# Optimization experiments

Measured on AMD Instinct MI355X. Metric: run time of the kernel, lower is better.

Reference implementation:

```python
import jax, jax.numpy as jnp
import numpy as np

B, T, I, H, FUT = 16384, 50, 6, 128, 30


def setup_inputs() -> dict:
    key = jax.random.key(0)
    ks = jax.random.split(key, 10)
    bound = 1.0 / np.sqrt(H)
    u = lambda k, shape: jax.random.uniform(k, shape, jnp.float32, -bound, bound)
    return {
        "history": jax.random.normal(ks[0], (B, T, I), jnp.float32),
        # GRU weights (PyTorch layout: gates stacked [r, z, n])
        "w_ih": u(ks[1], (3 * H, I)),
        "w_hh": u(ks[2], (3 * H, H)),
        "b_ih": u(ks[3], (3 * H,)),
        "b_hh": u(ks[4], (3 * H,)),
        # MLP head: Linear(H,H) -> ReLU -> Linear(H,I)
        "w1": u(ks[5], (H, H)),
        "b1": u(ks[6], (H,)),
        "w2": u(ks[7], (I, H)),
        "b2": u(ks[8], (I,)),
    }


def _gru_cell(h, x, w_ih, w_hh, b_ih, b_hh):
    # PyTorch GRU cell: gates ordered r, z, n
    gi = x @ w_ih.T + b_ih          # (B, 3H)
    gh = h @ w_hh.T + b_hh          # (B, 3H)
    i_r, i_z, i_n = jnp.split(gi, 3, axis=-1)
    h_r, h_z, h_n = jnp.split(gh, 3, axis=-1)
    r = jax.nn.sigmoid(i_r + h_r)
    z = jax.nn.sigmoid(i_z + h_z)
    n = jnp.tanh(i_n + r * h_n)
    return (1.0 - z) * n + z * h


def reference(history, w_ih, w_hh, b_ih, b_hh, w1, b1, w2, b2):
    # --- encode history: scan GRU over time ---
    h0 = jnp.zeros((history.shape[0], H), history.dtype)

    def enc_step(h, x_t):
        return _gru_cell(h, x_t, w_ih, w_hh, b_ih, b_hh), None

    h_last, _ = jax.lax.scan(enc_step, h0, jnp.swapaxes(history, 0, 1))  # (B, H)

    def head(h):
        return jax.nn.relu(h @ w1.T + b1) @ w2.T + b2  # (B, I)

    def dec_step(carry, _):
        h, x = carry
        h = _gru_cell(h, x, w_ih, w_hh, b_ih, b_hh)
        x = head(h)
        return (h, x), x

    x0 = history[:, -1]  # (B, I)
    _, preds = jax.lax.scan(dec_step, (h_last, x0), None, length=FUT)  # (FUT, B, I)
    return jnp.swapaxes(preds, 0, 1)  # (B, FUT, I)
```

## Files before the change

kernel.cpp:

```cpp
#include <hip/hip_runtime.h>

typedef _Float16 half8 __attribute__((ext_vector_type(8)));
typedef _Float16 half4 __attribute__((ext_vector_type(4)));
typedef float f32x4 __attribute__((ext_vector_type(4)));
typedef int int4v __attribute__((ext_vector_type(4)));

#define ROWS 64
#define HP 136
#define HBUFSZ (ROWS * HP)
#define LOG2E 1.442695041f
#define MFMA(a,b,c) __builtin_amdgcn_mfma_f32_16x16x32_f16((a),(b),(c),0,0,0)

__global__ __launch_bounds__(512, 2)
void traj_gru(const float* __restrict__ history,
              const float* __restrict__ w_ih, const float* __restrict__ w_hh,
              const float* __restrict__ b_ih, const float* __restrict__ b_hh,
              const float* __restrict__ w1, const float* __restrict__ b1,
              const float* __restrict__ w2, const float* __restrict__ b2,
              float* __restrict__ out)
{
    __shared__ __align__(16) _Float16 hbuf[2 * HBUFSZ];
    __shared__ __align__(16) _Float16 xhist[50 * ROWS * 6];
    __shared__ __align__(16) _Float16 xdec[ROWS * 8];
    __shared__ __align__(16) _Float16 w2f[4 * 4 * 16 * 8];

    const int tid  = threadIdx.x;
    const int wave = tid >> 6;
    const int lane = tid & 63;
    const int ln16 = lane & 15;
    const int q    = lane >> 4;
    const int sw   = ln16 & 3;
    const int rowbase = blockIdx.x * ROWS;
    const int dbase = wave * 16;
    const int bblk  = wave >> 1;
    const int colin = ((wave & 1) << 4) | ln16;

    for (int i = tid; i < 2 * HBUFSZ; i += 512) hbuf[i] = (_Float16)0;
    for (int i = tid; i < ROWS * 8; i += 512) xdec[i] = (_Float16)0;
    for (int i = tid; i < 4 * 4 * 16 * 8; i += 512) w2f[i] = (_Float16)0;
    __syncthreads();
    for (int idx = tid; idx < ROWS * 300; idx += 512) {
        int r = idx / 300, rem = idx - r * 300;
        int t = rem / 6, c = rem - t * 6;
        xhist[(t * ROWS + r) * 6 + c] = (_Float16)history[(rowbase + r) * 300 + rem];
    }
    if (tid < ROWS) xdec[tid * 8 + 6] = (_Float16)1.0f;
    for (int idx = tid; idx < 6 * 128; idx += 512) {
        int n = idx >> 7, k = idx & 127;
        int kt = k >> 5, qq = (k >> 3) & 3, j = k & 7;
        w2f[((kt * 4 + qq) * 16 + n) * 8 + j] = (_Float16)w2[n * 128 + k];
    }

    half8 Wg[3][4];
    #pragma unroll
    for (int g = 0; g < 3; ++g) {
        float sc = (g < 2) ? -LOG2E : -2.0f * LOG2E;
        #pragma unroll
        for (int kt = 0; kt < 4; ++kt) {
            const float* p = w_hh + (g * 128 + dbase + ln16) * 128 + kt * 32 + q * 8;
            half8 v;
            #pragma unroll
            for (int j = 0; j < 8; ++j) v[j] = (_Float16)(p[j] * sc);
            Wg[g][kt] = v;
        }
    }
    half8 Wx[3];
    #pragma unroll
    for (int g = 0; g < 3; ++g) {
        float sc = (g < 2) ? -LOG2E : -2.0f * LOG2E;
        half8 v;
        #pragma unroll
        for (int j = 0; j < 8; ++j) v[j] = (_Float16)0.0f;
        if (q == 0) {
            #pragma unroll
            for (int j = 0; j < 6; ++j) v[j] = (_Float16)(w_ih[(g * 128 + dbase + ln16) * 6 + j] * sc);
        }
        Wx[g] = v;
    }
    f32x4 brr, brz, bin, bhn;
    #pragma unroll
    for (int i = 0; i < 4; ++i) {
        int d = dbase + q * 4 + i;
        brr[i] = (b_ih[d]       + b_hh[d]      ) * (-LOG2E);
        brz[i] = (b_ih[128 + d] + b_hh[128 + d]) * (-LOG2E);
        bin[i] = b_ih[256 + d] * (-2.0f * LOG2E);
        bhn[i] = b_hh[256 + d] * (-2.0f * LOG2E);
    }
    half8 Bw1[4];
    #pragma unroll
    for (int kt = 0; kt < 4; ++kt) {
        const float* p = w1 + (dbase + ln16) * 128 + kt * 32 + q * 8;
        half8 v;
        #pragma unroll
        for (int j = 0; j < 8; ++j) v[j] = (_Float16)p[j];
        Bw1[kt] = v;
    }
    const float b1r = b1[dbase + ln16];
    const float b2r = (ln16 < 6) ? b2[ln16] : 0.0f;

    float hp[4][4] = {};

    __syncthreads();

    auto gru_step = [&](int p, int t, bool enc) {
        const _Float16* hb = hbuf + p * HBUFSZ;
        _Float16*       hn = hbuf + (p ^ 1) * HBUFSZ;
        half8 Bf[2][4], Bx[2];
        f32x4 ar[2], az[2], ahh[2], an[2];

        auto loadB = [&](int c, int buf) {
            const _Float16* rp = hb + (c * 16 + ln16) * HP;
            #pragma unroll
            for (int kt = 0; kt < 4; ++kt)
                Bf[buf][kt] = *(const half8*)(rp + kt * 32 + q * 8);
            if (enc) {
                const int* xi = (const int*)xhist;
                int base = (t * ROWS + c * 16 + ln16) * 3;
                int4v d = { xi[base], xi[base + 1], xi[base + 2], 0x3C00 };
                Bx[buf] = __builtin_bit_cast(half8, d);
            } else {
                Bx[buf] = *(const half8*)(xdec + (c * 16 + ln16) * 8);
            }
        };
        auto mfmas = [&](int buf) {
            f32x4 r = brr, z = brz, hh = bhn, n = bin;
            #pragma unroll
            for (int kt = 0; kt < 4; ++kt) {
                r  = MFMA(Wg[0][kt], Bf[buf][kt], r);
                z  = MFMA(Wg[1][kt], Bf[buf][kt], z);
                hh = MFMA(Wg[2][kt], Bf[buf][kt], hh);
            }
            r = MFMA(Wx[0], Bx[buf], r);
            z = MFMA(Wx[1], Bx[buf], z);
            n = MFMA(Wx[2], Bx[buf], n);
            ar[buf] = r; az[buf] = z; ahh[buf] = hh; an[buf] = n;
        };
        auto gates = [&](int c, int cb) {
            half4 hv;
            #pragma unroll
            for (int i = 0; i < 4; ++i) {
                float r = __builtin_amdgcn_rcpf(1.0f + __builtin_amdgcn_exp2f(ar[cb][i]));
                float z = __builtin_amdgcn_rcpf(1.0f + __builtin_amdgcn_exp2f(az[cb][i]));
                float tt = an[cb][i] + r * ahh[cb][i];
                float n = 2.0f * __builtin_amdgcn_rcpf(1.0f + __builtin_amdgcn_exp2f(tt)) - 1.0f;
                float h = n + z * (hp[c][i] - n);
                hp[c][i] = h;
                hv[i] = (_Float16)h;
            }
            *(half4*)(hn + (c * 16 + ln16) * HP + dbase + q * 4) = hv;
        };

        loadB(0, 0); mfmas(0);
        #pragma unroll
        for (int c = 0; c < 4; ++c) {
            const int cb = c & 1;
            if (c < 3) { loadB(c + 1, cb ^ 1); mfmas(cb ^ 1); }
            gates(c, cb);
        }
        __syncthreads();
    };

    auto head_step = [&](int f, int p) {
        const _Float16* hb = hbuf + p * HBUFSZ;
        _Float16*       a1 = hbuf + (p ^ 1) * HBUFSZ;
        half8 Ah[2][4];
        f32x4 aa[2];
        auto loadA = [&](int c, int buf) {
            const _Float16* rp = hb + (c * 16 + ln16) * HP;
            #pragma unroll
            for (int kt = 0; kt < 4; ++kt)
                Ah[buf][kt] = *(const half8*)(rp + kt * 32 + q * 8);
        };
        auto mfh = [&](int buf) {
            f32x4 a = {0,0,0,0};
            #pragma unroll
            for (int kt = 0; kt < 4; ++kt) a = MFMA(Ah[buf][kt], Bw1[kt], a);
            aa[buf] = a;
        };
        auto relu4 = [&](int c, int cb) {
            #pragma unroll
            for (int i = 0; i < 4; ++i) {
                float v = aa[cb][i] + b1r;
                v = v > 0.0f ? v : 0.0f;
                a1[(c * 16 + q * 4 + i) * HP + ((bblk ^ i) << 5) + colin] = (_Float16)v;
            }
        };
        loadA(0, 0); mfh(0);
        #pragma unroll
        for (int c = 0; c < 4; ++c) {
            const int cb = c & 1;
            if (c < 3) { loadA(c + 1, cb ^ 1); mfh(cb ^ 1); }
            relu4(c, cb);
        }
        __syncthreads();
        if (wave < 4) {
            const _Float16* rp = a1 + (wave * 16 + ln16) * HP;
            f32x4 o = {0,0,0,0};
            #pragma unroll
            for (int kt = 0; kt < 4; ++kt) {
                half8 Aa = *(const half8*)(rp + ((kt ^ sw) << 5) + q * 8);
                half8 Bw = *(const half8*)&w2f[((kt * 4 + q) * 16 + ln16) * 8];
                o = MFMA(Aa, Bw, o);
            }
            if (ln16 < 6) {
                #pragma unroll
                for (int i = 0; i < 4; ++i) {
                    int row = wave * 16 + q * 4 + i;
                    float v = o[i] + b2r;
                    out[(rowbase + row) * 180 + f * 6 + ln16] = v;
                    xdec[row * 8 + ln16] = (_Float16)v;
                }
            }
        }
        __syncthreads();
    };

    int p = 0;
    #pragma unroll 1
    for (int t = 0; t < 50; ++t) { gru_step(p, t, true); p ^= 1; }
    #pragma unroll 1
    for (int f = 0; f < 30; ++f) {
        gru_step(p, f == 0 ? 49 : 0, f == 0);
        p ^= 1;
        head_step(f, p);
    }
}

extern "C" void kernel_launch(void* const* d_in, const int* in_sizes, int n_in,
                              void* d_out, int out_size, void* d_ws, size_t ws_size,
                              hipStream_t stream) {
    (void)in_sizes; (void)n_in; (void)d_ws; (void)ws_size; (void)out_size;
    traj_gru<<<dim3(16384 / ROWS), dim3(512), 0, stream>>>(
        (const float*)d_in[0], (const float*)d_in[1], (const float*)d_in[2],
        (const float*)d_in[3], (const float*)d_in[4], (const float*)d_in[5],
        (const float*)d_in[6], (const float*)d_in[7], (const float*)d_in[8],
        (float*)d_out);
}
```

Before: 273.8 us.

## Split GRU work 2x4 over batch halves and hidden groups, stage w1 in LDS

Waves are regrouped so each one handles half the batch rows (two 16-row chunks) and a 32-wide hidden slice (two M-tiles), in place of all 64 rows for a 16-wide slice. This halves the LDS reads of the hidden state per wave and doubles the reuse of each loaded B fragment across two weight tiles. The gate biases are folded into the constant-1 column of the input MFMA so the accumulators start at zero. w1 now lives in LDS and is reloaded every head step rather than held in registers. In exchange, per-thread weight registers double (Wg is now 24 half8) and there is less software pipelining across chunks, which at launch bounds (512,2) may cause spills or lower occupancy.

```diff
diff --git a/kernel.cpp b/kernel.cpp
--- a/kernel.cpp
+++ b/kernel.cpp
@@ -23,17 +23,16 @@
     __shared__ __align__(16) _Float16 xhist[50 * ROWS * 6];
     __shared__ __align__(16) _Float16 xdec[ROWS * 8];
     __shared__ __align__(16) _Float16 w2f[4 * 4 * 16 * 8];
+    __shared__ __align__(16) _Float16 w1f[4 * 4 * 128 * 8];
 
     const int tid  = threadIdx.x;
     const int wave = tid >> 6;
     const int lane = tid & 63;
     const int ln16 = lane & 15;
     const int q    = lane >> 4;
-    const int sw   = ln16 & 3;
+    const int bh   = wave >> 2;
+    const int dg   = wave & 3;
     const int rowbase = blockIdx.x * ROWS;
-    const int dbase = wave * 16;
-    const int bblk  = wave >> 1;
-    const int colin = ((wave & 1) << 4) | ln16;
 
     for (int i = tid; i < 2 * HBUFSZ; i += 512) hbuf[i] = (_Float16)0;
     for (int i = tid; i < ROWS * 8; i += 512) xdec[i] = (_Float16)0;
@@ -50,55 +49,63 @@
         int kt = k >> 5, qq = (k >> 3) & 3, j = k & 7;
         w2f[((kt * 4 + qq) * 16 + n) * 8 + j] = (_Float16)w2[n * 128 + k];
     }
-
-    half8 Wg[3][4];
+    for (int idx = tid; idx < 16384; idx += 512) {
+        int j = idx & 7, d = (idx >> 3) & 127, fq = idx >> 10;
+        int kt = fq >> 2, qq = fq & 3;
+        w1f[idx] = (_Float16)w1[d * 128 + kt * 32 + qq * 8 + j];
+    }
+
+    half8 Wg[3][4][2];
     #pragma unroll
     for (int g = 0; g < 3; ++g) {
         float sc = (g < 2) ? -LOG2E : -2.0f * LOG2E;
         #pragma unroll
-        for (int kt = 0; kt < 4; ++kt) {
-            const float* p = w_hh + (g * 128 + dbase + ln16) * 128 + kt * 32 + q * 8;
-            half8 v;
-            #pragma unroll
-            for (int j = 0; j < 8; ++j) v[j] = (_Float16)(p[j] * sc);
-            Wg[g][kt] = v;
-        }
-    }
-    half8 Wx[3];
+        for (int mt = 0; mt < 2; ++mt) {
+            #pragma unroll
+            for (int kt = 0; kt < 4; ++kt) {
+                const float* p = w_hh + (g * 128 + dg * 32 + mt * 16 + ln16) * 128 + kt * 32 + q * 8;
+                half8 v;
+                #pragma unroll
+                for (int j = 0; j < 8; ++j) v[j] = (_Float16)(p[j] * sc);
+                Wg[g][kt][mt] = v;
+            }
+        }
+    }
+    half8 Wx[3][2];
     #pragma unroll
     for (int g = 0; g < 3; ++g) {
         float sc = (g < 2) ? -LOG2E : -2.0f * LOG2E;
-        half8 v;
-        #pragma unroll
-        for (int j = 0; j < 8; ++j) v[j] = (_Float16)0.0f;
-        if (q == 0) {
-            #pragma unroll
-            for (int j = 0; j < 6; ++j) v[j] = (_Float16)(w_ih[(g * 128 + dbase + ln16) * 6 + j] * sc);
-        }
-        Wx[g] = v;
-    }
-    f32x4 brr, brz, bin, bhn;
+        #pragma unroll
+        for (int mt = 0; mt < 2; ++mt) {
+            half8 v;
+            #pragma unroll
+            for (int j = 0; j < 8; ++j) v[j] = (_Float16)0.0f;
+            if (q == 0) {
+                int d = dg * 32 + mt * 16 + ln16;
+                #pragma unroll
+                for (int j = 0; j < 6; ++j) v[j] = (_Float16)(w_ih[(g * 128 + d) * 6 + j] * sc);
+                float bias;
+                if      (g == 0) bias = b_ih[d]       + b_hh[d];
+                else if (g == 1) bias = b_ih[128 + d] + b_hh[128 + d];
+                else             bias = b_ih[256 + d];
+                v[6] = (_Float16)(bias * sc);
+            }
+            Wx[g][mt] = v;
+        }
+    }
+    f32x4 bhn[2];
     #pragma unroll
-    for (int i = 0; i < 4; ++i) {
-        int d = dbase + q * 4 + i;
-        brr[i] = (b_ih[d]       + b_hh[d]      ) * (-LOG2E);
-        brz[i] = (b_ih[128 + d] + b_hh[128 + d]) * (-LOG2E);
-        bin[i] = b_ih[256 + d] * (-2.0f * LOG2E);
-        bhn[i] = b_hh[256 + d] * (-2.0f * LOG2E);
-    }
-    half8 Bw1[4];
-    #pragma unroll
-    for (int kt = 0; kt < 4; ++kt) {
-        const float* p = w1 + (dbase + ln16) * 128 + kt * 32 + q * 8;
-        half8 v;
-        #pragma unroll
-        for (int j = 0; j < 8; ++j) v[j] = (_Float16)p[j];
-        Bw1[kt] = v;
-    }
-    const float b1r = b1[dbase + ln16];
+    for (int mt = 0; mt < 2; ++mt)
+        #pragma unroll
+        for (int i = 0; i < 4; ++i)
+            bhn[mt][i] = b_hh[256 + dg * 32 + mt * 16 + q * 4 + i] * (-2.0f * LOG2E);
+
+    float b1rv[2];
+    b1rv[0] = b1[dg * 32 + ln16];
+    b1rv[1] = b1[dg * 32 + 16 + ln16];
     const float b2r = (ln16 < 6) ? b2[ln16] : 0.0f;
 
-    float hp[4][4] = {};
+    float hp[2][2][4] = {};
 
     __syncthreads();
 
@@ -106,101 +113,110 @@
         const _Float16* hb = hbuf + p * HBUFSZ;
         _Float16*       hn = hbuf + (p ^ 1) * HBUFSZ;
         half8 Bf[2][4], Bx[2];
-        f32x4 ar[2], az[2], ahh[2], an[2];
-
-        auto loadB = [&](int c, int buf) {
+
+        auto loadB = [&](int c2) {
+            int c = 2 * bh + c2;
             const _Float16* rp = hb + (c * 16 + ln16) * HP;
             #pragma unroll
             for (int kt = 0; kt < 4; ++kt)
-                Bf[buf][kt] = *(const half8*)(rp + kt * 32 + q * 8);
+                Bf[c2][kt] = *(const half8*)(rp + kt * 32 + q * 8);
             if (enc) {
                 const int* xi = (const int*)xhist;
                 int base = (t * ROWS + c * 16 + ln16) * 3;
-                int4v d = { xi[base], xi[base + 1], xi[base + 2], 0x3C00 };
-                Bx[buf] = __builtin_bit_cast(half8, d);
+                int4v dv = { xi[base], xi[base + 1], xi[base + 2], 0x3C00 };
+                Bx[c2] = __builtin_bit_cast(half8, dv);
             } else {
-                Bx[buf] = *(const half8*)(xdec + (c * 16 + ln16) * 8);
+                Bx[c2] = *(const half8*)(xdec + (c * 16 + ln16) * 8);
             }
         };
-        auto mfmas = [&](int buf) {
-            f32x4 r = brr, z = brz, hh = bhn, n = bin;
-            #pragma unroll
-            for (int kt = 0; kt < 4; ++kt) {
-                r  = MFMA(Wg[0][kt], Bf[buf][kt], r);
-                z  = MFMA(Wg[1][kt], Bf[buf][kt], z);
-                hh = MFMA(Wg[2][kt], Bf[buf][kt], hh);
-            }
-            r = MFMA(Wx[0], Bx[buf], r);
-            z = MFMA(Wx[1], Bx[buf], z);
-            n = MFMA(Wx[2], Bx[buf], n);
-            ar[buf] = r; az[buf] = z; ahh[buf] = hh; an[buf] = n;
+        auto mfmas = [&](int c2, f32x4 (&A)[2][4]) {
+            #pragma unroll
+            for (int mt = 0; mt < 2; ++mt) {
+                f32x4 r = {0,0,0,0}, z = {0,0,0,0}, n = {0,0,0,0}, hh = bhn[mt];
+                #pragma unroll
+                for (int kt = 0; kt < 4; ++kt) {
+                    r  = MFMA(Wg[0][kt][mt], Bf[c2][kt], r);
+                    z  = MFMA(Wg[1][kt][mt], Bf[c2][kt], z);
+                    hh = MFMA(Wg[2][kt][mt], Bf[c2][kt], hh);
+                }
+                r = MFMA(Wx[0][mt], Bx[c2], r);
+                z = MFMA(Wx[1][mt], Bx[c2], z);
+                n = MFMA(Wx[2][mt], Bx[c2], n);
+                A[mt][0] = r; A[mt][1] = z; A[mt][2] = hh; A[mt][3] = n;
+            }
         };
-        auto gates = [&](int c, int cb) {
-            half4 hv;
-            #pragma unroll
-            for (int i = 0; i < 4; ++i) {
-                float r = __builtin_amdgcn_rcpf(1.0f + __builtin_amdgcn_exp2f(ar[cb][i]));
-                float z = __builtin_amdgcn_rcpf(1.0f + __builtin_amdgcn_exp2f(az[cb][i]));
-                float tt = an[cb][i] + r * ahh[cb][i];
-                float n = 2.0f * __builtin_amdgcn_rcpf(1.0f + __builtin_amdgcn_exp2f(tt)) - 1.0f;
-                float h = n + z * (hp[c][i] - n);
-                hp[c][i] = h;
-                hv[i] = (_Float16)h;
-            }
-            *(half4*)(hn + (c * 16 + ln16) * HP + dbase + q * 4) = hv;
+        auto gates = [&](int c2, f32x4 (&A)[2][4]) {
+            int c = 2 * bh + c2;
+            #pragma unroll
+            for (int mt = 0; mt < 2; ++mt) {
+                half4 hv;
+                #pragma unroll
+                for (int i = 0; i < 4; ++i) {
+                    float rr = __builtin_amdgcn_rcpf(1.0f + __builtin_amdgcn_exp2f(A[mt][0][i]));
+                    float zz = __builtin_amdgcn_rcpf(1.0f + __builtin_amdgcn_exp2f(A[mt][1][i]));
+                    float tt = A[mt][3][i] + rr * A[mt][2][i];
+                    float nn = 2.0f * __builtin_amdgcn_rcpf(1.0f + __builtin_amdgcn_exp2f(tt)) - 1.0f;
+                    float h = nn + zz * (hp[c2][mt][i] - nn);
+                    hp[c2][mt][i] = h;
+                    hv[i] = (_Float16)h;
+                }
+                *(half4*)(hn + (c * 16 + ln16) * HP + dg * 32 + mt * 16 + q * 4) = hv;
+            }
         };
 
-        loadB(0, 0); mfmas(0);
-        #pragma unroll
-        for (int c = 0; c < 4; ++c) {
-            const int cb = c & 1;
-            if (c < 3) { loadB(c + 1, cb ^ 1); mfmas(cb ^ 1); }
-            gates(c, cb);
-        }
+        f32x4 accA[2][4], accB[2][4];
+        loadB(0);
+        mfmas(0, accA);
+        loadB(1);
+        gates(0, accA);
+        mfmas(1, accB);
+        gates(1, accB);
         __syncthreads();
     };
 
     auto head_step = [&](int f, int p) {
         const _Float16* hb = hbuf + p * HBUFSZ;
-        _Float16*       a1 = hbuf + (p ^ 1) * HBUFSZ;
-        half8 Ah[2][4];
-        f32x4 aa[2];
-        auto loadA = [&](int c, int buf) {
+        _Float16*       a1s = hbuf + (p ^ 1) * HBUFSZ;
+        half8 Bw[4][2];
+        #pragma unroll
+        for (int kt = 0; kt < 4; ++kt)
+            #pragma unroll
+            for (int nt = 0; nt < 2; ++nt)
+                Bw[kt][nt] = *(const half8*)(w1f + ((kt * 4 + q) * 128 + dg * 32 + nt * 16 + ln16) * 8);
+        #pragma unroll
+        for (int c2 = 0; c2 < 2; ++c2) {
+            int c = 2 * bh + c2;
             const _Float16* rp = hb + (c * 16 + ln16) * HP;
+            half8 Ah[4];
             #pragma unroll
             for (int kt = 0; kt < 4; ++kt)
-                Ah[buf][kt] = *(const half8*)(rp + kt * 32 + q * 8);
-        };
-        auto mfh = [&](int buf) {
-            f32x4 a = {0,0,0,0};
-            #pragma unroll
-            for (int kt = 0; kt < 4; ++kt) a = MFMA(Ah[buf][kt], Bw1[kt], a);
-            aa[buf] = a;
-        };
-        auto relu4 = [&](int c, int cb) {
+                Ah[kt] = *(const half8*)(rp + kt * 32 + q * 8);
+            f32x4 a0 = {0,0,0,0}, a1v = {0,0,0,0};
+            #pragma unroll
+            for (int kt = 0; kt < 4; ++kt) {
+                a0  = MFMA(Ah[kt], Bw[kt][0], a0);
+                a1v = MFMA(Ah[kt], Bw[kt][1], a1v);
+            }
             #pragma unroll
             for (int i = 0; i < 4; ++i) {
-                float v = aa[cb][i] + b1r;
-                v = v > 0.0f ? v : 0.0f;
-                a1[(c * 16 + q * 4 + i) * HP + ((bblk ^ i) << 5) + colin] = (_Float16)v;
-            }
-        };
-        loadA(0, 0); mfh(0);
-        #pragma unroll
-        for (int c = 0; c < 4; ++c) {
-            const int cb = c & 1;
-            if (c < 3) { loadA(c + 1, cb ^ 1); mfh(cb ^ 1); }
-            relu4(c, cb);
+                float v0 = a0[i] + b1rv[0];
+                v0 = v0 > 0.0f ? v0 : 0.0f;
+                a1s[(c * 16 + q * 4 + i) * HP + ((dg ^ i) << 5) + ln16] = (_Float16)v0;
+                float v1 = a1v[i] + b1rv[1];
+                v1 = v1 > 0.0f ? v1 : 0.0f;
+                a1s[(c * 16 + q * 4 + i) * HP + ((dg ^ i) << 5) + 16 + ln16] = (_Float16)v1;
+            }
         }
         __syncthreads();
         if (wave < 4) {
-            const _Float16* rp = a1 + (wave * 16 + ln16) * HP;
+            const int sw = ln16 & 3;
+            const _Float16* rp = a1s + (wave * 16 + ln16) * HP;
             f32x4 o = {0,0,0,0};
             #pragma unroll
             for (int kt = 0; kt < 4; ++kt) {
                 half8 Aa = *(const half8*)(rp + ((kt ^ sw) << 5) + q * 8);
-                half8 Bw = *(const half8*)&w2f[((kt * 4 + q) * 16 + ln16) * 8];
-                o = MFMA(Aa, Bw, o);
+                half8 Bw2 = *(const half8*)&w2f[((kt * 4 + q) * 16 + ln16) * 8];
+                o = MFMA(Aa, Bw2, o);
             }
             if (ln16 < 6) {
                 #pragma unroll
```

After: 272.2 us, median of 2. About the same (-0.6%).
